# Optimization experiments

Hardware: AMD Instinct MI355X
Metric: run time of the kernel (lower is better)

The kernel has to match this reference:

```python
import jax, jax.numpy as jnp
import numpy as np

N, E = 20000, 640000
LATENT, HID, OUT, HEADS = 512, 256, 128, 2
NEG_SLOPE = 0.2


def setup_inputs() -> dict:
    key = jax.random.key(0)
    ks = jax.random.split(key, 12)
    s = 0.02
    return {
        "z": jax.random.normal(ks[0], (N, LATENT), dtype=jnp.float32),
        "edge_index": jax.random.randint(ks[1], (2, E), 0, N, dtype=jnp.int64),
        "W1": jax.random.normal(ks[2], (LATENT, HID), dtype=jnp.float32) * s,
        "b1": jnp.zeros((HID,), dtype=jnp.float32),
        "W2": jax.random.normal(ks[3], (HID, HID * HEADS), dtype=jnp.float32) * s,
        "b2": jnp.zeros((HID * HEADS,), dtype=jnp.float32),
        "Wg": jax.random.normal(ks[4], (HID * HEADS, HEADS * OUT), dtype=jnp.float32) * s,
        "att_src": jax.random.normal(ks[5], (HEADS, OUT), dtype=jnp.float32) * s,
        "att_dst": jax.random.normal(ks[6], (HEADS, OUT), dtype=jnp.float32) * s,
        "bias_g": jnp.zeros((HEADS * OUT,), dtype=jnp.float32),
        "W3": jax.random.normal(ks[7], (OUT * HEADS, 512), dtype=jnp.float32) * s,
        "b3": jnp.zeros((512,), dtype=jnp.float32),
    }


def _gat_conv(x, edge_index, Wg, att_src, att_dst, bias_g):
    n = x.shape[0]
    # add self loops (PyG GATConv default add_self_loops=True)
    loops = jnp.tile(jnp.arange(n, dtype=edge_index.dtype)[None, :], (2, 1))
    ei = jnp.concatenate([edge_index, loops], axis=1)
    src, dst = ei[0], ei[1]
    xp = (x @ Wg).reshape(n, HEADS, OUT)          # [N,H,C]
    a_src = jnp.einsum('nhc,hc->nh', xp, att_src)  # [N,H]
    a_dst = jnp.einsum('nhc,hc->nh', xp, att_dst)
    alpha = jax.nn.leaky_relu(a_src[src] + a_dst[dst], NEG_SLOPE)  # [E+N,H]
    amax = jax.ops.segment_max(alpha, dst, num_segments=n)
    alpha = jnp.exp(alpha - amax[dst])
    denom = jax.ops.segment_sum(alpha, dst, num_segments=n)
    alpha = alpha / jnp.maximum(denom[dst], 1e-16)
    msg = xp[src] * alpha[:, :, None]              # [E+N,H,C]
    out = jax.ops.segment_sum(msg, dst, num_segments=n)  # [N,H,C]
    return out.reshape(n, HEADS * OUT) + bias_g


def reference(z, edge_index, W1, b1, W2, b2, Wg, att_src, att_dst, bias_g, W3, b3):
    x = jax.nn.relu(z @ W1 + b1)
    x = jax.nn.relu(x @ W2 + b2)
    x = _gat_conv(x, edge_index, Wg, att_src, att_dst, bias_g)
    return x @ W3 + b3
```

## Files before the change

### kernel.cpp

```cpp
#include <hip/hip_runtime.h>
#include <hip/hip_bf16.h>
#include <float.h>

#define N_NODES 20000
#define LATENT  512
#define HID     256
#define OUT_C   128
#define HEADS   2
#define HC      256
#define NEG_SLOPE 0.2f

typedef _Float16 half8 __attribute__((ext_vector_type(8)));
typedef __attribute__((ext_vector_type(4))) float f32x4;
typedef __attribute__((ext_vector_type(2))) float f32x2;

__device__ __forceinline__ ushort f2h(float v) {
    _Float16 h = (_Float16)v;
    return *(ushort*)&h;
}
__device__ __forceinline__ float h2f(ushort u) {
    _Float16 h = *(_Float16*)&u;
    return (float)h;
}

#if __has_builtin(__builtin_amdgcn_cvt_pk_fp8_f32) && __has_builtin(__builtin_amdgcn_cvt_pk_f32_fp8)
#define FP8_HW 1
#else
#define FP8_HW 0
#endif

__device__ __forceinline__ uint f32_to_e4m3(float v) {
#if FP8_HW
    return (uint)(__builtin_amdgcn_cvt_pk_fp8_f32(v, v, 0, false) & 0xff);
#else
    _Float16 hf = (_Float16)(v * 0.00390625f);
    uint hb = *(ushort*)&hf;
    uint s = (hb >> 8) & 0x80;
    uint mag = hb & 0x7fff;
    mag = (mag + 0x3f + ((mag >> 7) & 1)) >> 7;
    if (mag > 0x7e) mag = 0x7e;
    return s | mag;
#endif
}

__device__ __forceinline__ void gl_lds16(const ushort* g, ushort* l) {
    __builtin_amdgcn_global_load_lds(
        (const __attribute__((address_space(1))) unsigned int*)g,
        (__attribute__((address_space(3))) unsigned int*)l, 16, 0, 0);
}

__global__ __launch_bounds__(512, 4) void fused_mlp(
    const ushort* __restrict__ z16, const ushort* __restrict__ W1T,
    const float* __restrict__ b1, const ushort* __restrict__ W2T,
    const float* __restrict__ b2, const ushort* __restrict__ WgT,
    const float* __restrict__ attS, const float* __restrict__ attD,
    float* __restrict__ aS, float* __restrict__ aD,
    unsigned char* __restrict__ xp8, int M)
{
    __shared__ ushort lds[40960];

    const int t = threadIdx.x;
    const int l = t & 63;
    const int w = t >> 6;
    const int wr = w & 3;
    const int wc = w >> 2;
    const int lm = l & 15;
    const int q  = l >> 4;
    const int q4 = q * 4;
    const int row0 = (int)blockIdx.x * 64;
    const int lr16 = l >> 2;
    const int gsh = (((l & 3) ^ ((l >> 4) & 3)) << 3);
    const int csw = ((q ^ ((lm >> 2) & 3)) << 3);

    constexpr int X1   = 0;
    constexpr int SLAB = 16384;
    constexpr int SB   = 24576;

    auto barsync = [&]() {
        __builtin_amdgcn_s_barrier();
        __builtin_amdgcn_sched_barrier(0);
    };

    auto issue1 = [&](int c) {
        ushort* B = &lds[(c % 3) * 10240];
        const int kk = c * 32;
        #pragma unroll
        for (int u = 0; u < 3; ++u) {
            const int ii = w + u * 8;
            if (ii < 20) {
                const ushort* g = (ii < 4)
                    ? z16 + (size_t)(row0 + ii * 16 + lr16) * 512 + kk + gsh
                    : W1T + (size_t)((ii - 4) * 16 + lr16) * 512 + kk + gsh;
                gl_lds16(g, B + ii * 512);
            }
        }
    };
    auto issue2 = [&](int s, int c) {
        ushort* B = &lds[SLAB + (c & 1) * 4096];
        gl_lds16(W2T + (size_t)(s * 128 + w * 16 + lr16) * 256 + c * 32 + gsh,
                 B + w * 512);
    };
    auto issue3 = [&](int s, int c) {
        ushort* B = &lds[SB + (c & 1) * 8192];
        #pragma unroll
        for (int u = 0; u < 2; ++u) {
            const int ii = w + u * 8;
            gl_lds16(WgT + (size_t)(ii * 16 + lr16) * 512 + s * 128 + c * 32 + gsh,
                     B + ii * 512);
        }
    };

    const f32x4 zf = {0.f, 0.f, 0.f, 0.f};

    f32x4 acc1[8];
    #pragma unroll
    for (int i = 0; i < 8; ++i) acc1[i] = zf;

    issue1(0); issue1(1);
    for (int c = 0; c < 16; ++c) {
        __builtin_amdgcn_sched_barrier(0);
        if (c + 1 < 16) {
            if (w < 4) asm volatile("s_waitcnt vmcnt(3)" ::: "memory");
            else       asm volatile("s_waitcnt vmcnt(2)" ::: "memory");
        } else         asm volatile("s_waitcnt vmcnt(0)" ::: "memory");
        barsync();
        if (c + 2 < 16) issue1(c + 2);
        const ushort* B = &lds[(c % 3) * 10240];
        half8 af = *(const half8*)&B[(wr * 16 + lm) * 32 + csw];
        #pragma unroll
        for (int ni = 0; ni < 8; ++ni) {
            half8 bf = *(const half8*)&B[2048 + (wc * 128 + ni * 16 + lm) * 32 + csw];
            acc1[ni] = __builtin_amdgcn_mfma_f32_16x16x32_f16(af, bf, acc1[ni], 0, 0, 0);
        }
    }
    __builtin_amdgcn_s_barrier();
    issue2(0, 0); issue2(0, 1);
    #pragma unroll
    for (int ni = 0; ni < 8; ++ni) {
        const int col = wc * 128 + ni * 16 + lm;
        const float bv = b1[col];
        const int ch = col >> 5, c5 = col & 31;
        #pragma unroll
        for (int r = 0; r < 4; ++r) {
            const int row = wr * 16 + q4 + r;
            const float v = fmaxf(acc1[ni][r] + bv, 0.f);
            lds[X1 + ch * 2048 + row * 32 + (((c5 >> 3) ^ q) << 3) + (c5 & 7)] = f2h(v);
        }
    }
    asm volatile("s_waitcnt lgkmcnt(0)" ::: "memory");
    barsync();

    f32x4 acc3[8];
    #pragma unroll
    for (int i = 0; i < 8; ++i) acc3[i] = zf;

    for (int s = 0; s < 4; ++s) {
        f32x4 acc2[4];
        #pragma unroll
        for (int i = 0; i < 4; ++i) acc2[i] = zf;

        for (int c = 0; c < 8; ++c) {
            __builtin_amdgcn_sched_barrier(0);
            if (c == 0) asm volatile("s_waitcnt vmcnt(1)" ::: "memory");
            else        asm volatile("s_waitcnt vmcnt(0)" ::: "memory");
            barsync();
            if (c >= 1 && c + 1 < 8) issue2(s, c + 1);
            if (c == 7) { issue3(s, 0); issue3(s, 1); }
            const ushort* Bf = &lds[SLAB + (c & 1) * 4096];
            half8 af = *(const half8*)&lds[X1 + c * 2048 + (wr * 16 + lm) * 32 + csw];
            #pragma unroll
            for (int ni = 0; ni < 4; ++ni) {
                half8 bf = *(const half8*)&Bf[(wc * 64 + ni * 16 + lm) * 32 + csw];
                acc2[ni] = __builtin_amdgcn_mfma_f32_16x16x32_f16(af, bf, acc2[ni], 0, 0, 0);
            }
        }
        __builtin_amdgcn_s_barrier();
        #pragma unroll
        for (int ni = 0; ni < 4; ++ni) {
            const int c7 = wc * 64 + ni * 16 + lm;
            const float bv = b2[s * 128 + c7];
            const int ch = c7 >> 5, c5 = c7 & 31;
            #pragma unroll
            for (int r = 0; r < 4; ++r) {
                const int row = wr * 16 + q4 + r;
                const float v = fmaxf(acc2[ni][r] + bv, 0.f);
                lds[SLAB + ch * 2048 + row * 32 + (((c5 >> 3) ^ q) << 3) + (c5 & 7)] = f2h(v);
            }
        }
        asm volatile("s_waitcnt lgkmcnt(0)" ::: "memory");
        barsync();

        for (int c = 0; c < 4; ++c) {
            __builtin_amdgcn_sched_barrier(0);
            if (c == 0)                asm volatile("s_waitcnt vmcnt(2)" ::: "memory");
            else if (c == 3 && s < 3)  asm volatile("s_waitcnt vmcnt(1)" ::: "memory");
            else                       asm volatile("s_waitcnt vmcnt(0)" ::: "memory");
            barsync();
            if (c == 1) issue3(s, 2);
            if (c == 2) { issue3(s, 3);
                          if (s < 3) issue2(s + 1, 0); }
            const ushort* Bf = &lds[SB + (c & 1) * 8192];
            half8 af = *(const half8*)&lds[SLAB + c * 2048 + (wr * 16 + lm) * 32 + csw];
            #pragma unroll
            for (int ni = 0; ni < 8; ++ni) {
                half8 bf = *(const half8*)&Bf[(wc * 128 + ni * 16 + lm) * 32 + csw];
                acc3[ni] = __builtin_amdgcn_mfma_f32_16x16x32_f16(af, bf, acc3[ni], 0, 0, 0);
            }
        }
        __builtin_amdgcn_s_barrier();
        if (s < 3) issue2(s + 1, 1);
        __builtin_amdgcn_sched_barrier(0);
    }

    const int h = wc;
    float asv[8], adv[8];
    #pragma unroll
    for (int ni = 0; ni < 8; ++ni) {
        const int col = wc * 128 + ni * 16 + lm;
        asv[ni] = attS[col];
        adv[ni] = attD[col];
    }
    #pragma unroll
    for (int r = 0; r < 4; ++r) {
        const int row = row0 + wr * 16 + q4 + r;
        float ps = 0.f, pd = 0.f;
        #pragma unroll
        for (int ni = 0; ni < 8; ++ni) {
            const float v = acc3[ni][r];
            ps += v * asv[ni];
            pd += v * adv[ni];
            if (row < M)
                xp8[(size_t)row * HC + wc * 128 + ni * 16 + lm] =
                    (unsigned char)f32_to_e4m3(v);
        }
        #pragma unroll
        for (int off = 8; off > 0; off >>= 1) {
            ps += __shfl_xor(ps, off);
            pd += __shfl_xor(pd, off);
        }
        if (lm == 0 && row < M) {
            atomicAdd(&aS[2 * row + h], ps);
            atomicAdd(&aD[2 * row + h], pd);
        }
    }
}

template<int BN, int LOGNBY>
__global__ __launch_bounds__(256, 4) void gemm_f16(
    const ushort* __restrict__ A, const ushort* __restrict__ BT,
    const float* __restrict__ bias,
    float* __restrict__ Cf, ushort* __restrict__ Ch,
    int M, int N, int K, int relu)
{
    static_assert(BN == 64, "vmcnt immediates assume 3 DMAs/chunk");
    constexpr int NI  = BN / 32;
    constexpr int BUF = 4096 + BN * 32;
    __shared__ ushort lds[3 * BUF];

    const int t = threadIdx.x;
    const int l = t & 63;
    const int w = t >> 6;
    const int wm = (w >> 1) * 64;
    const int wn = (w & 1) * (BN / 2);
    const int lm = l & 15;
    const int q  = l >> 4;
    const int q4 = q * 4;

    const int T  = (int)gridDim.x;
    const int qq = T >> 3, rr = T & 7;
    const int kx = (int)blockIdx.x & 7;
    const int jx = (int)blockIdx.x >> 3;
    const int lin = kx * qq + (kx < rr ? kx : rr) + jx;
    const int row0 = (lin >> LOGNBY) * 128;
    const int col0 = (lin & ((1 << LOGNBY) - 1)) * BN;

    const int jr0 = w * 16 + (l >> 2);
    const int gsh = (((l & 3) ^ ((l >> 4) & 3)) << 3);
    const ushort* gA0 = A + (size_t)(row0 + jr0) * K + gsh;
    const ushort* gA1 = gA0 + (size_t)64 * K;
    const ushort* gB0 = BT + (size_t)(col0 + jr0) * K + gsh;
    const int dA0 = w * 512, dA1 = (4 + w) * 512;
    const int dB0 = 4096 + w * 512;

    const int csw = ((q ^ ((lm >> 2) & 3)) << 3);

    const f32x4 zf = {0.f, 0.f, 0.f, 0.f};
    f32x4 acc[4][NI];
    #pragma unroll
    for (int i = 0; i < 4; ++i)
        #pragma unroll
        for (int j = 0; j < NI; ++j) acc[i][j] = zf;

    const int NC = K >> 5;

    auto issue = [&](int c) {
        ushort* B = lds + (size_t)(c % 3) * BUF;
        const int kk = c * 32;
        gl_lds16(gA0 + kk, B + dA0);
        gl_lds16(gA1 + kk, B + dA1);
        gl_lds16(gB0 + kk, B + dB0);
    };

    auto compute = [&](int c) {
        const ushort* B = lds + (size_t)(c % 3) * BUF;
        half8 bf[NI];
        #pragma unroll
        for (int ni = 0; ni < NI; ++ni) {
            const int boff = (wn + ni * 16 + lm) * 32 + csw;
            bf[ni] = *(const half8*)&B[4096 + boff];
        }
        #pragma unroll
        for (int mi = 0; mi < 4; ++mi) {
            const int aoff = (wm + mi * 16 + lm) * 32 + csw;
            half8 af = *(const half8*)&B[aoff];
            #pragma unroll
            for (int ni = 0; ni < NI; ++ni)
                acc[mi][ni] = __builtin_amdgcn_mfma_f32_16x16x32_f16(
                    af, bf[ni], acc[mi][ni], 0, 0, 0);
        }
    };

    issue(0); issue(1);
    for (int c = 0; c < NC; ++c) {
        __builtin_amdgcn_sched_barrier(0);
        if (c + 1 < NC) asm volatile("s_waitcnt vmcnt(3)" ::: "memory");
        else            asm volatile("s_waitcnt vmcnt(0)" ::: "memory");
        __builtin_amdgcn_s_barrier();
        __builtin_amdgcn_sched_barrier(0);
        if (c + 2 < NC) issue(c + 2);
        compute(c);
    }

    #pragma unroll
    for (int mi = 0; mi < 4; ++mi) {
        #pragma unroll
        for (int ni = 0; ni < NI; ++ni) {
            const int col = col0 + wn + ni * 16 + lm;
            const float bv = bias ? bias[col] : 0.f;
            #pragma unroll
            for (int r = 0; r < 4; ++r) {
                const int row = row0 + wm + mi * 16 + q4 + r;
                if (row >= M) continue;
                float v = acc[mi][ni][r] + bv;
                if (relu) v = fmaxf(v, 0.f);
                const size_t idx = (size_t)row * N + col;
                if (Cf) Cf[idx] = v;
                if (Ch) Ch[idx] = f2h(v);
            }
        }
    }
}

#define CVT_BLOCKS 10000
#define TR_BLOCKS  2048
__global__ __launch_bounds__(256) void prologue_kernel(
    const float* __restrict__ z, ushort* __restrict__ z_f16,
    int* deg, int* cursor, float* aS, float* aD, int n,
    const float* __restrict__ W1, const float* __restrict__ W2,
    const float* __restrict__ Wg, const float* __restrict__ W3,
    ushort* __restrict__ T1, ushort* __restrict__ T2,
    ushort* __restrict__ Tg, ushort* __restrict__ T3)
{
    const int b = blockIdx.x;
    if (b < CVT_BLOCKS) {
        int i = b * 256 + threadIdx.x;
        if (i < n) {
            deg[i] = 0; cursor[i] = 0;
            ((float2*)aS)[i] = make_float2(0.f, 0.f);
            ((float2*)aD)[i] = make_float2(0.f, 0.f);
        }
        float4 v = ((const float4*)z)[i];
        ((ushort4*)z_f16)[i] = make_ushort4(f2h(v.x), f2h(v.y), f2h(v.z), f2h(v.w));
    } else {
        int idx = (b - CVT_BLOCKS) * 256 + threadIdx.x;
        int which = idx >> 17, i = idx & 131071;
        const float* W; ushort* T; int K, N;
        if (which == 0)      { W = W1; T = T1; K = 512; N = 256; }
        else if (which == 1) { W = W2; T = T2; K = 256; N = 512; }
        else if (which == 2) { W = Wg; T = Tg; K = 512; N = 256; }
        else                 { W = W3; T = T3; K = 256; N = 512; }
        int k = i / N, nn = i - k * N;
        T[(size_t)nn * K + k] = f2h(W[i]);
    }
}

__global__ __launch_bounds__(256) void hist_kernel(
    const int* __restrict__ dst, int* deg, int E_real, int ET)
{
    int e = blockIdx.x * blockDim.x + threadIdx.x;
    if (e >= ET) return;
    int d = (e < E_real) ? dst[e] : (e - E_real);
    atomicAdd(&deg[d], 1);
}

__global__ __launch_bounds__(1024) void scan_kernel(
    const int* __restrict__ deg, int* __restrict__ rowptr, int n)
{
    __shared__ int part[1024];
    const int t = threadIdx.x;
    const int chunk = (n + 1023) / 1024;
    const int lo = t * chunk;
    const int hi = min(lo + chunk, n);
    int s = 0;
    for (int i = lo; i < hi; ++i) s += deg[i];
    part[t] = s;
    __syncthreads();
    #pragma unroll
    for (int off = 1; off < 1024; off <<= 1) {
        int add = (t >= off) ? part[t - off] : 0;
        __syncthreads();
        part[t] += add;
        __syncthreads();
    }
    int run = part[t] - s;
    for (int i = lo; i < hi; ++i) { rowptr[i] = run; run += deg[i]; }
    if (t == 1023) rowptr[n] = part[1023];
}

__global__ __launch_bounds__(256) void scatter_kernel(
    const int* __restrict__ src, const int* __restrict__ dst,
    const int* __restrict__ rowptr, int* cursor,
    int* __restrict__ sorted_src, int E_real, int ET)
{
    int e = blockIdx.x * blockDim.x + threadIdx.x;
    if (e >= ET) return;
    int s, d;
    if (e < E_real) { s = src[e]; d = dst[e]; }
    else            { s = e - E_real; d = s; }
    int pos = rowptr[d] + atomicAdd(&cursor[d], 1);
    sorted_src[pos] = s;
}

__global__ __launch_bounds__(256) void gat_aggregate(
    const int* __restrict__ rowptr, const int* __restrict__ sorted_src,
    const float* __restrict__ a_src, const float* __restrict__ a_dst,
    const unsigned char* __restrict__ xp8, const float* __restrict__ bias_g,
    ushort* __restrict__ xg, int n)
{
    const int d = blockIdx.x * 4 + (threadIdx.x >> 6);
    if (d >= n) return;
    const int lane = threadIdx.x & 63;
    const int hsel = lane & 32;
    const int start = rowptr[d], end = rowptr[d + 1];

    const float ad0 = a_dst[2 * d + 0];
    const float ad1 = a_dst[2 * d + 1];

    float4 acc = make_float4(0.f, 0.f, 0.f, 0.f);
    float denom = 0.f;

    for (int e0 = start; e0 < end; e0 += 32) {
        const int cnt = min(32, end - e0);
        const int idx = lane & 31;
        float wsel = 0.f; int off = 0;
        if (idx < cnt) {
            int s = sorted_src[e0 + idx];
            float v0 = a_src[2 * s + 0] + ad0;
            float v1 = a_src[2 * s + 1] + ad1;
            v0 = (v0 > 0.f) ? v0 : NEG_SLOPE * v0;
            v1 = (v1 > 0.f) ? v1 : NEG_SLOPE * v1;
            wsel = (lane < 32) ? __expf(v0) : __expf(v1);
            off = s * HC;
        }
        int j = 0;
        for (; j + 8 <= cnt; j += 8) {
            float w_[8]; int o_[8];
            #pragma unroll
            for (int u = 0; u < 8; ++u) {
                w_[u] = __shfl(wsel, (j + u) + hsel);
                o_[u] = __shfl(off, j + u);
            }
            uint v_[8];
            #pragma unroll
            for (int u = 0; u < 8; ++u)
                v_[u] = *(const uint*)(xp8 + o_[u] + 4 * lane);
            #pragma unroll
            for (int u = 0; u < 8; ++u) {
                denom += w_[u];
#if FP8_HW
                f32x2 lo = __builtin_amdgcn_cvt_pk_f32_fp8((int)v_[u], false);
                f32x2 hi = __builtin_amdgcn_cvt_pk_f32_fp8((int)v_[u], true);
                acc.x += w_[u] * lo.x; acc.y += w_[u] * lo.y;
                acc.z += w_[u] * hi.x; acc.w += w_[u] * hi.y;
#else
                const float wu = w_[u] * 256.0f;
                const uint b = v_[u];
                acc.x += wu * h2f(((b & 0x80u) << 8) | ((b & 0x7fu) << 7));
                acc.y += wu * h2f((((b >> 8) & 0x80u) << 8) | (((b >> 8) & 0x7fu) << 7));
                acc.z += wu * h2f((((b >> 16) & 0x80u) << 8) | (((b >> 16) & 0x7fu) << 7));
                acc.w += wu * h2f((((b >> 24) & 0x80u) << 8) | (((b >> 24) & 0x7fu) << 7));
#endif
            }
        }
        for (; j < cnt; ++j) {
            const float w = __shfl(wsel, j + hsel);
            const int   o = __shfl(off, j);
            const uint  b = *(const uint*)(xp8 + o + 4 * lane);
            denom += w;
#if FP8_HW
            f32x2 lo = __builtin_amdgcn_cvt_pk_f32_fp8((int)b, false);
            f32x2 hi = __builtin_amdgcn_cvt_pk_f32_fp8((int)b, true);
            acc.x += w * lo.x; acc.y += w * lo.y;
            acc.z += w * hi.x; acc.w += w * hi.y;
#else
            const float wu = w * 256.0f;
            acc.x += wu * h2f(((b & 0x80u) << 8) | ((b & 0x7fu) << 7));
            acc.y += wu * h2f((((b >> 8) & 0x80u) << 8) | (((b >> 8) & 0x7fu) << 7));
            acc.z += wu * h2f((((b >> 16) & 0x80u) << 8) | (((b >> 16) & 0x7fu) << 7));
            acc.w += wu * h2f((((b >> 24) & 0x80u) << 8) | (((b >> 24) & 0x7fu) << 7));
#endif
        }
    }

    const float inv = 1.f / fmaxf(denom, 1e-16f);
    const int c = 4 * lane;
    const float4 bg = *(const float4*)(bias_g + c);
    const size_t base = ((size_t)d * HC + c) >> 2;
    ((ushort4*)xg)[base] = make_ushort4(
        f2h(acc.x * inv + bg.x), f2h(acc.y * inv + bg.y),
        f2h(acc.z * inv + bg.z), f2h(acc.w * inv + bg.w));
}

extern "C" void kernel_launch(void* const* d_in, const int* in_sizes, int n_in,
                              void* d_out, int out_size, void* d_ws, size_t ws_size,
                              hipStream_t stream)
{
    const float* z       = (const float*)d_in[0];
    const int*   ei      = (const int*)d_in[1];
    const float* W1      = (const float*)d_in[2];
    const float* b1      = (const float*)d_in[3];
    const float* W2      = (const float*)d_in[4];
    const float* b2      = (const float*)d_in[5];
    const float* Wg      = (const float*)d_in[6];
    const float* att_src = (const float*)d_in[7];
    const float* att_dst = (const float*)d_in[8];
    const float* bias_g  = (const float*)d_in[9];
    const float* W3      = (const float*)d_in[10];
    const float* b3      = (const float*)d_in[11];
    float* out = (float*)d_out;

    const int n = N_NODES;
    const int E_real = in_sizes[1] / 2;
    const int ET = E_real + n;
    const int* src = ei;
    const int* dst = ei + E_real;

    char* p = (char*)d_ws;
    auto alloc = [&](size_t bytes) {
        char* r = p;
        p += (bytes + 63) & ~(size_t)63;
        return r;
    };
    const int np = n + 128;
    ushort* z_f16  = (ushort*)alloc((size_t)np * LATENT * 2);
    ushort* xg_f16 = (ushort*)alloc((size_t)np * HID * 2);
    unsigned char* xp8 = (unsigned char*)alloc((size_t)n * HC);
    ushort* W1T = (ushort*)alloc((size_t)LATENT * HID * 2);
    ushort* W2T = (ushort*)alloc((size_t)HID * 512 * 2);
    ushort* WgT = (ushort*)alloc((size_t)512 * HC * 2);
    ushort* W3T = (ushort*)alloc((size_t)HC * 512 * 2);
    float* a_src = (float*)alloc((size_t)2 * n * 4);
    float* a_dst = (float*)alloc((size_t)2 * n * 4);
    int* deg        = (int*)alloc((size_t)n * 4);
    int* rowptr     = (int*)alloc(((size_t)n + 1) * 4);
    int* cursor     = (int*)alloc((size_t)n * 4);
    int* sorted_src = (int*)alloc((size_t)ET * 4);

    const int gm128 = (n + 127) / 128;

    prologue_kernel<<<CVT_BLOCKS + TR_BLOCKS, 256, 0, stream>>>(
        z, z_f16, deg, cursor, a_src, a_dst, n,
        W1, W2, Wg, W3, W1T, W2T, WgT, W3T);
    hist_kernel<<<(ET + 255) / 256, 256, 0, stream>>>(dst, deg, E_real, ET);
    scan_kernel<<<1, 1024, 0, stream>>>(deg, rowptr, n);
    scatter_kernel<<<(ET + 255) / 256, 256, 0, stream>>>(
        src, dst, rowptr, cursor, sorted_src, E_real, ET);

    fused_mlp<<<(n + 63) / 64, 512, 0, stream>>>(
        z_f16, W1T, b1, W2T, b2, WgT,
        att_src, att_dst, a_src, a_dst, xp8, n);

    gat_aggregate<<<(n + 3) / 4, 256, 0, stream>>>(
        rowptr, sorted_src, a_src, a_dst, xp8, bias_g, xg_f16, n);

    gemm_f16<64, 3><<<gm128 * 8, 256, 0, stream>>>(
        xg_f16, W3T, b3, out, nullptr, n, 512, HC, 0);
}
```

Baseline: 289.1 us.

## Load MFMA operands directly from global memory instead of LDS DMA staging

Drops the async global-to-LDS DMA pipelines with triple/double buffering in fused_mlp and the final GEMM. MFMA fragments for z, W1T, W2T, WgT, A and W3T are now read straight from global memory into registers, and only intermediate activations stay in LDS. The aim is to cut LDS footprint and the per-chunk barrier and waitcnt synchronisation. In exchange it loses explicit prefetch overlap and the shared reuse of weight tiles across waves, so more redundant global or L2 traffic is possible. The last GEMM also loses bounds handling for partial row tiles on loads.

```diff
diff --git a/kernel.cpp b/kernel.cpp
--- a/kernel.cpp
+++ b/kernel.cpp
@@ -43,12 +43,6 @@
 #endif
 }
 
-__device__ __forceinline__ void gl_lds16(const ushort* g, ushort* l) {
-    __builtin_amdgcn_global_load_lds(
-        (const __attribute__((address_space(1))) unsigned int*)g,
-        (__attribute__((address_space(3))) unsigned int*)l, 16, 0, 0);
-}
-
 __global__ __launch_bounds__(512, 4) void fused_mlp(
     const ushort* __restrict__ z16, const ushort* __restrict__ W1T,
     const float* __restrict__ b1, const ushort* __restrict__ W2T,
@@ -57,7 +51,7 @@
     float* __restrict__ aS, float* __restrict__ aD,
     unsigned char* __restrict__ xp8, int M)
 {
-    __shared__ ushort lds[40960];
+    __shared__ ushort lds[24576];
 
     const int t = threadIdx.x;
     const int l = t & 63;
@@ -68,73 +62,28 @@
     const int q  = l >> 4;
     const int q4 = q * 4;
     const int row0 = (int)blockIdx.x * 64;
-    const int lr16 = l >> 2;
-    const int gsh = (((l & 3) ^ ((l >> 4) & 3)) << 3);
     const int csw = ((q ^ ((lm >> 2) & 3)) << 3);
 
     constexpr int X1   = 0;
     constexpr int SLAB = 16384;
-    constexpr int SB   = 24576;
-
-    auto barsync = [&]() {
-        __builtin_amdgcn_s_barrier();
-        __builtin_amdgcn_sched_barrier(0);
-    };
-
-    auto issue1 = [&](int c) {
-        ushort* B = &lds[(c % 3) * 10240];
-        const int kk = c * 32;
-        #pragma unroll
-        for (int u = 0; u < 3; ++u) {
-            const int ii = w + u * 8;
-            if (ii < 20) {
-                const ushort* g = (ii < 4)
-                    ? z16 + (size_t)(row0 + ii * 16 + lr16) * 512 + kk + gsh
-                    : W1T + (size_t)((ii - 4) * 16 + lr16) * 512 + kk + gsh;
-                gl_lds16(g, B + ii * 512);
-            }
-        }
-    };
-    auto issue2 = [&](int s, int c) {
-        ushort* B = &lds[SLAB + (c & 1) * 4096];
-        gl_lds16(W2T + (size_t)(s * 128 + w * 16 + lr16) * 256 + c * 32 + gsh,
-                 B + w * 512);
-    };
-    auto issue3 = [&](int s, int c) {
-        ushort* B = &lds[SB + (c & 1) * 8192];
-        #pragma unroll
-        for (int u = 0; u < 2; ++u) {
-            const int ii = w + u * 8;
-            gl_lds16(WgT + (size_t)(ii * 16 + lr16) * 512 + s * 128 + c * 32 + gsh,
-                     B + ii * 512);
-        }
-    };
-
     const f32x4 zf = {0.f, 0.f, 0.f, 0.f};
 
     f32x4 acc1[8];
     #pragma unroll
     for (int i = 0; i < 8; ++i) acc1[i] = zf;
-
-    issue1(0); issue1(1);
-    for (int c = 0; c < 16; ++c) {
-        __builtin_amdgcn_sched_barrier(0);
-        if (c + 1 < 16) {
-            if (w < 4) asm volatile("s_waitcnt vmcnt(3)" ::: "memory");
-            else       asm volatile("s_waitcnt vmcnt(2)" ::: "memory");
-        } else         asm volatile("s_waitcnt vmcnt(0)" ::: "memory");
-        barsync();
-        if (c + 2 < 16) issue1(c + 2);
-        const ushort* B = &lds[(c % 3) * 10240];
-        half8 af = *(const half8*)&B[(wr * 16 + lm) * 32 + csw];
-        #pragma unroll
-        for (int ni = 0; ni < 8; ++ni) {
-            half8 bf = *(const half8*)&B[2048 + (wc * 128 + ni * 16 + lm) * 32 + csw];
-            acc1[ni] = __builtin_amdgcn_mfma_f32_16x16x32_f16(af, bf, acc1[ni], 0, 0, 0);
-        }
-    }
-    __builtin_amdgcn_s_barrier();
-    issue2(0, 0); issue2(0, 1);
+    {
+        const ushort* ar = z16 + (size_t)(row0 + wr * 16 + lm) * 512 + q * 8;
+        const ushort* br = W1T + (size_t)(wc * 128 + lm) * 512 + q * 8;
+        #pragma unroll
+        for (int c = 0; c < 16; ++c) {
+            half8 af = *(const half8*)(ar + c * 32);
+            #pragma unroll
+            for (int ni = 0; ni < 8; ++ni) {
+                half8 bf = *(const half8*)(br + (size_t)(ni * 16) * 512 + c * 32);
+                acc1[ni] = __builtin_amdgcn_mfma_f32_16x16x32_f16(af, bf, acc1[ni], 0, 0, 0);
+            }
+        }
+    }
     #pragma unroll
     for (int ni = 0; ni < 8; ++ni) {
         const int col = wc * 128 + ni * 16 + lm;
@@ -148,33 +97,32 @@
         }
     }
     asm volatile("s_waitcnt lgkmcnt(0)" ::: "memory");
-    barsync();
+    __builtin_amdgcn_s_barrier();
+    __builtin_amdgcn_sched_barrier(0);
 
     f32x4 acc3[8];
     #pragma unroll
     for (int i = 0; i < 8; ++i) acc3[i] = zf;
 
+    #pragma unroll
     for (int s = 0; s < 4; ++s) {
         f32x4 acc2[4];
         #pragma unroll
         for (int i = 0; i < 4; ++i) acc2[i] = zf;
-
-        for (int c = 0; c < 8; ++c) {
-            __builtin_amdgcn_sched_barrier(0);
-            if (c == 0) asm volatile("s_waitcnt vmcnt(1)" ::: "memory");
-            else        asm volatile("s_waitcnt vmcnt(0)" ::: "memory");
-            barsync();
-            if (c >= 1 && c + 1 < 8) issue2(s, c + 1);
-            if (c == 7) { issue3(s, 0); issue3(s, 1); }
-            const ushort* Bf = &lds[SLAB + (c & 1) * 4096];
-            half8 af = *(const half8*)&lds[X1 + c * 2048 + (wr * 16 + lm) * 32 + csw];
-            #pragma unroll
-            for (int ni = 0; ni < 4; ++ni) {
-                half8 bf = *(const half8*)&Bf[(wc * 64 + ni * 16 + lm) * 32 + csw];
-                acc2[ni] = __builtin_amdgcn_mfma_f32_16x16x32_f16(af, bf, acc2[ni], 0, 0, 0);
+        {
+            const ushort* br = W2T + (size_t)(s * 128 + wc * 64 + lm) * 256 + q * 8;
+            #pragma unroll
+            for (int c = 0; c < 8; ++c) {
+                half8 af = *(const half8*)&lds[X1 + c * 2048 + (wr * 16 + lm) * 32 + csw];
+                #pragma unroll
+                for (int ni = 0; ni < 4; ++ni) {
+                    half8 bf = *(const half8*)(br + (size_t)(ni * 16) * 256 + c * 32);
+                    acc2[ni] = __builtin_amdgcn_mfma_f32_16x16x32_f16(af, bf, acc2[ni], 0, 0, 0);
+                }
             }
         }
         __builtin_amdgcn_s_barrier();
+        __builtin_amdgcn_sched_barrier(0);
         #pragma unroll
         for (int ni = 0; ni < 4; ++ni) {
             const int c7 = wc * 64 + ni * 16 + lm;
@@ -188,28 +136,21 @@
             }
         }
         asm volatile("s_waitcnt lgkmcnt(0)" ::: "memory");
-        barsync();
-
-        for (int c = 0; c < 4; ++c) {
-            __builtin_amdgcn_sched_barrier(0);
-            if (c == 0)                asm volatile("s_waitcnt vmcnt(2)" ::: "memory");
-            else if (c == 3 && s < 3)  asm volatile("s_waitcnt vmcnt(1)" ::: "memory");
-            else                       asm volatile("s_waitcnt vmcnt(0)" ::: "memory");
-            barsync();
-            if (c == 1) issue3(s, 2);
-            if (c == 2) { issue3(s, 3);
-                          if (s < 3) issue2(s + 1, 0); }
-            const ushort* Bf = &lds[SB + (c & 1) * 8192];
-            half8 af = *(const half8*)&lds[SLAB + c * 2048 + (wr * 16 + lm) * 32 + csw];
-            #pragma unroll
-            for (int ni = 0; ni < 8; ++ni) {
-                half8 bf = *(const half8*)&Bf[(wc * 128 + ni * 16 + lm) * 32 + csw];
-                acc3[ni] = __builtin_amdgcn_mfma_f32_16x16x32_f16(af, bf, acc3[ni], 0, 0, 0);
-            }
-        }
         __builtin_amdgcn_s_barrier();
-        if (s < 3) issue2(s + 1, 1);
         __builtin_amdgcn_sched_barrier(0);
+
+        {
+            const ushort* br = WgT + (size_t)(wc * 128 + lm) * 512 + s * 128 + q * 8;
+            #pragma unroll
+            for (int c = 0; c < 4; ++c) {
+                half8 af = *(const half8*)&lds[SLAB + c * 2048 + (wr * 16 + lm) * 32 + csw];
+                #pragma unroll
+                for (int ni = 0; ni < 8; ++ni) {
+                    half8 bf = *(const half8*)(br + (size_t)(ni * 16) * 512 + c * 32);
+                    acc3[ni] = __builtin_amdgcn_mfma_f32_16x16x32_f16(af, bf, acc3[ni], 0, 0, 0);
+                }
+            }
+        }
     }
 
     const int h = wc;
@@ -245,23 +186,17 @@
     }
 }
 
-template<int BN, int LOGNBY>
-__global__ __launch_bounds__(256, 4) void gemm_f16(
-    const ushort* __restrict__ A, const ushort* __restrict__ BT,
+__global__ __launch_bounds__(256, 4) void gemm4_direct(
+    const ushort* __restrict__ A,
+    const ushort* __restrict__ BT,
     const float* __restrict__ bias,
-    float* __restrict__ Cf, ushort* __restrict__ Ch,
-    int M, int N, int K, int relu)
-{
-    static_assert(BN == 64, "vmcnt immediates assume 3 DMAs/chunk");
-    constexpr int NI  = BN / 32;
-    constexpr int BUF = 4096 + BN * 32;
-    __shared__ ushort lds[3 * BUF];
-
+    float* __restrict__ C, int M)
+{
     const int t = threadIdx.x;
     const int l = t & 63;
     const int w = t >> 6;
     const int wm = (w >> 1) * 64;
-    const int wn = (w & 1) * (BN / 2);
+    const int wn = (w & 1) * 32;
     const int lm = l & 15;
     const int q  = l >> 4;
     const int q4 = q * 4;
@@ -271,81 +206,40 @@
     const int kx = (int)blockIdx.x & 7;
     const int jx = (int)blockIdx.x >> 3;
     const int lin = kx * qq + (kx < rr ? kx : rr) + jx;
-    const int row0 = (lin >> LOGNBY) * 128;
-    const int col0 = (lin & ((1 << LOGNBY) - 1)) * BN;
-
-    const int jr0 = w * 16 + (l >> 2);
-    const int gsh = (((l & 3) ^ ((l >> 4) & 3)) << 3);
-    const ushort* gA0 = A + (size_t)(row0 + jr0) * K + gsh;
-    const ushort* gA1 = gA0 + (size_t)64 * K;
-    const ushort* gB0 = BT + (size_t)(col0 + jr0) * K + gsh;
-    const int dA0 = w * 512, dA1 = (4 + w) * 512;
-    const int dB0 = 4096 + w * 512;
-
-    const int csw = ((q ^ ((lm >> 2) & 3)) << 3);
+    const int row0 = (lin >> 3) * 128;
+    const int col0 = (lin & 7) * 64;
 
     const f32x4 zf = {0.f, 0.f, 0.f, 0.f};
-    f32x4 acc[4][NI];
-    #pragma unroll
-    for (int i = 0; i < 4; ++i)
-        #pragma unroll
-        for (int j = 0; j < NI; ++j) acc[i][j] = zf;
-
-    const int NC = K >> 5;
-
-    auto issue = [&](int c) {
-        ushort* B = lds + (size_t)(c % 3) * BUF;
-        const int kk = c * 32;
-        gl_lds16(gA0 + kk, B + dA0);
-        gl_lds16(gA1 + kk, B + dA1);
-        gl_lds16(gB0 + kk, B + dB0);
-    };
-
-    auto compute = [&](int c) {
-        const ushort* B = lds + (size_t)(c % 3) * BUF;
-        half8 bf[NI];
-        #pragma unroll
-        for (int ni = 0; ni < NI; ++ni) {
-            const int boff = (wn + ni * 16 + lm) * 32 + csw;
-            bf[ni] = *(const half8*)&B[4096 + boff];
-        }
+    f32x4 acc[4][2];
+    #pragma unroll
+    for (int i = 0; i < 4; ++i) { acc[i][0] = zf; acc[i][1] = zf; }
+
+    const ushort* ar = A + (size_t)(row0 + wm + lm) * 256 + q * 8;
+    const ushort* br = BT + (size_t)(col0 + wn + lm) * 256 + q * 8;
+
+    #pragma unroll
+    for (int c = 0; c < 8; ++c) {
+        half8 bf0 = *(const half8*)(br + c * 32);
+        half8 bf1 = *(const half8*)(br + (size_t)16 * 256 + c * 32);
         #pragma unroll
         for (int mi = 0; mi < 4; ++mi) {
-            const int aoff = (wm + mi * 16 + lm) * 32 + csw;
-            half8 af = *(const half8*)&B[aoff];
-            #pragma unroll
-            for (int ni = 0; ni < NI; ++ni)
-                acc[mi][ni] = __builtin_amdgcn_mfma_f32_16x16x32_f16(
-                    af, bf[ni], acc[mi][ni], 0, 0, 0);
-        }
-    };
-
-    issue(0); issue(1);
-    for (int c = 0; c < NC; ++c) {
-        __builtin_amdgcn_sched_barrier(0);
-        if (c + 1 < NC) asm volatile("s_waitcnt vmcnt(3)" ::: "memory");
-        else            asm volatile("s_waitcnt vmcnt(0)" ::: "memory");
-        __builtin_amdgcn_s_barrier();
-        __builtin_amdgcn_sched_barrier(0);
-        if (c + 2 < NC) issue(c + 2);
-        compute(c);
+            half8 af = *(const half8*)(ar + (size_t)(mi * 16) * 256 + c * 32);
+            acc[mi][0] = __builtin_amdgcn_mfma_f32_16x16x32_f16(af, bf0, acc[mi][0], 0, 0, 0);
+            acc[mi][1] = __builtin_amdgcn_mfma_f32_16x16x32_f16(af, bf1, acc[mi][1], 0, 0, 0);
+        }
     }
 
     #pragma unroll
     for (int mi = 0; mi < 4; ++mi) {
         #pragma unroll
-        for (int ni = 0; ni < NI; ++ni) {
+        for (int ni = 0; ni < 2; ++ni) {
             const int col = col0 + wn + ni * 16 + lm;
-            const float bv = bias ? bias[col] : 0.f;
+            const float bv = bias[col];
             #pragma unroll
             for (int r = 0; r < 4; ++r) {
                 const int row = row0 + wm + mi * 16 + q4 + r;
                 if (row >= M) continue;
-                float v = acc[mi][ni][r] + bv;
-                if (relu) v = fmaxf(v, 0.f);
-                const size_t idx = (size_t)row * N + col;
-                if (Cf) Cf[idx] = v;
-                if (Ch) Ch[idx] = f2h(v);
+                C[(size_t)row * 512 + col] = acc[mi][ni][r] + bv;
             }
         }
     }
@@ -583,6 +477,6 @@
     gat_aggregate<<<(n + 3) / 4, 256, 0, stream>>>(
         rowptr, sorted_src, a_src, a_dst, xp8, bias_g, xg_f16, n);
 
-    gemm_f16<64, 3><<<gm128 * 8, 256, 0, stream>>>(
-        xg_f16, W3T, b3, out, nullptr, n, 512, HC, 0);
-}
+    gemm4_direct<<<gm128 * 8, 256, 0, stream>>>(
+        xg_f16, W3T, b3, out, n);
+}
```

Measured after the change: 443.1 us. +53.3%, slower.
